# Performance work log

Hardware: AMD Instinct MI355X
Metric: run time of the kernel (lower is better)

The kernel has to match this reference:

```python
import jax, jax.numpy as jnp
import numpy as np
import math

GOLDEN_CENTER = 1.0 / math.e
GOLDEN_LOWER = 0.5 - math.log(4.0 / 3.0)
GOLDEN_UPPER = 0.5

B, T, D = 4, 2048, 1024
E = 8
I = 4096 // (E // 2)  # expert_inter = 1024


def setup_inputs() -> dict:
    key = jax.random.key(0)
    k = jax.random.split(key, 6)
    s_d = 1.0 / math.sqrt(D)
    s_i = 1.0 / math.sqrt(I)
    return {
        "x": jax.random.normal(k[0], (B, T, D), jnp.float32),
        "Wg": jax.random.normal(k[1], (E, D, I), jnp.float32) * s_d,
        "Wu": jax.random.normal(k[2], (E, D, I), jnp.float32) * s_d,
        "Wd": jax.random.normal(k[3], (E, I, D), jnp.float32) * s_i,
        "Wr": jax.random.normal(k[4], (D, E), jnp.float32) * s_d,
        "temperature": jnp.ones((1,), jnp.float32),
    }


def _routing_weights(x, Wr, temperature):
    # inhibition: [B,T,E]
    inh = jax.nn.sigmoid((x @ Wr) / temperature)
    in_zone = (inh >= GOLDEN_LOWER) & (inh <= GOLDEN_UPPER)
    dist = jnp.abs(inh - GOLDEN_CENTER)
    w = jnp.exp(-dist / 0.1) * in_zone.astype(x.dtype)
    wsum = w.sum(axis=-1, keepdims=True)
    no_expert = wsum < 1e-8
    # fallback: softer decay, keep top-2 experts, renormalize
    fb = jnp.exp(-dist / 0.3)
    _, top2 = jax.lax.top_k(fb, 2)  # [B,T,2]
    fb_mask = jax.nn.one_hot(top2, E, dtype=x.dtype).sum(axis=-2)  # [B,T,E]
    fb_w = fb * fb_mask
    fb_w = fb_w / jnp.clip(fb_w.sum(axis=-1, keepdims=True), 1e-8)
    w = jnp.where(no_expert, fb_w, w)
    wsum = w.sum(axis=-1, keepdims=True)
    return w / jnp.clip(wsum, 1e-8)


def reference(x, Wg, Wu, Wd, Wr, temperature):
    weights = _routing_weights(x, Wr, temperature)  # [B,T,E]
    gate = jnp.einsum("btd,edi->beti", x, Wg)
    up = jnp.einsum("btd,edi->beti", x, Wu)
    h = jax.nn.silu(gate) * up  # [B,E,T,I]
    e_out = jnp.einsum("beti,eid->betd", h, Wd)
    out = jnp.einsum("bte,betd->btd", weights, e_out)
    return out
```

## Files before the change

kernel.cpp:

```cpp
#include <hip/hip_runtime.h>
#include <hip/hip_bf16.h>
#include <cstdint>

typedef __attribute__((ext_vector_type(8))) _Float16 f16x8;
typedef __attribute__((ext_vector_type(4))) _Float16 f16x4;
typedef __attribute__((ext_vector_type(4))) float f32x4;

#define GOLDEN_CENTER_F 0.36787944117144233f
#define GOLDEN_LOWER_F  0.21231792754821915f
#define GOLDEN_UPPER_F  0.5f

static constexpr int Dm = 1024;
static constexpr int Im = 1024;
static constexpr int NTOK = 8192;
static constexpr int NE = 8;

__device__ __forceinline__ void async16(const _Float16* g, _Float16* l) {
  __builtin_amdgcn_global_load_lds(
      (const __attribute__((address_space(1))) void*)g,
      (__attribute__((address_space(3))) void*)l,
      16, 0, 0);
}

__global__ void routing_kernel(const float* __restrict__ x, const float* __restrict__ Wr,
                               const float* __restrict__ temp, float* __restrict__ wts) {
  const int wave = threadIdx.x >> 6, lane = threadIdx.x & 63;
  const int t = blockIdx.x * 4 + wave;
  const float* xr = x + (size_t)t * Dm;
  float acc[NE] = {0.f,0.f,0.f,0.f,0.f,0.f,0.f,0.f};
  for (int d = lane; d < Dm; d += 64) {
    float xv = xr[d];
    const float* wr = Wr + (size_t)d * NE;
#pragma unroll
    for (int e = 0; e < NE; ++e) acc[e] += xv * wr[e];
  }
#pragma unroll
  for (int off = 32; off > 0; off >>= 1) {
#pragma unroll
    for (int e = 0; e < NE; ++e) acc[e] += __shfl_down(acc[e], off, 64);
  }
  if (lane == 0) {
    float T = temp[0];
    float w[NE], dist[NE];
    float wsum = 0.f;
#pragma unroll
    for (int e = 0; e < NE; ++e) {
      float inh = 1.f / (1.f + expf(-acc[e] / T));
      dist[e] = fabsf(inh - GOLDEN_CENTER_F);
      bool zone = (inh >= GOLDEN_LOWER_F) && (inh <= GOLDEN_UPPER_F);
      w[e] = zone ? expf(-dist[e] / 0.1f) : 0.f;
      wsum += w[e];
    }
    if (wsum < 1e-8f) {
      float fb[NE];
#pragma unroll
      for (int e = 0; e < NE; ++e) fb[e] = expf(-dist[e] / 0.3f);
      int i1 = 0;
      for (int e = 1; e < NE; ++e) if (fb[e] > fb[i1]) i1 = e;
      int i2 = (i1 == 0) ? 1 : 0;
      for (int e = 0; e < NE; ++e) if (e != i1 && fb[e] > fb[i2]) i2 = e;
      float s = fmaxf(fb[i1] + fb[i2], 1e-8f);
#pragma unroll
      for (int e = 0; e < NE; ++e) w[e] = 0.f;
      w[i1] = fb[i1] / s;
      w[i2] = fb[i2] / s;
      wsum = w[i1] + w[i2];
    }
    float inv = 1.f / fmaxf(wsum, 1e-8f);
#pragma unroll
    for (int e = 0; e < NE; ++e) wts[(size_t)t * NE + e] = w[e] * inv;
  }
}

__global__ void compact_kernel(const float* __restrict__ wts, int* __restrict__ tok,
                               float* __restrict__ wc, int* __restrict__ cnt,
                               int* __restrict__ pos) {
  const int e = blockIdx.x;
  const int tid = threadIdx.x;
  const int wave = tid >> 6, lane = tid & 63;
  __shared__ int wcnt[4];
  __shared__ int s_running;
  if (tid == 0) s_running = 0;
  __syncthreads();
  for (int base = 0; base < NTOK; base += 256) {
    int t = base + tid;
    float w = wts[(size_t)t * NE + e];
    bool act = w > 0.f;
    unsigned long long mask = __ballot(act);
    int prefix = __popcll(mask & ((1ull << lane) - 1ull));
    if (lane == 0) wcnt[wave] = __popcll(mask);
    __syncthreads();
    int wbase = 0;
    for (int i = 0; i < wave; ++i) wbase += wcnt[i];
    int run = s_running;
    int p = run + wbase + prefix;
    pos[(size_t)t * NE + e] = act ? p : -1;
    if (act) {
      tok[(size_t)e * NTOK + p] = t;
      wc[(size_t)e * NTOK + p] = w;
    }
    __syncthreads();
    if (tid == 0) s_running = run + wcnt[0] + wcnt[1] + wcnt[2] + wcnt[3];
    __syncthreads();
  }
  int c = s_running;
  if (tid == 0) cnt[e] = c;
  int padded = (c + 127) & ~127;
  for (int p = c + tid; p < padded; p += 256) {
    tok[(size_t)e * NTOK + p] = 0;
    wc[(size_t)e * NTOK + p] = 0.f;
  }
}

__global__ void cvt_x_kernel(const float* __restrict__ x, _Float16* __restrict__ xb) {
  size_t i = ((size_t)blockIdx.x * 256 + threadIdx.x) * 4;
  float4 v = *(const float4*)(x + i);
  f16x4 o = {(_Float16)v.x, (_Float16)v.y, (_Float16)v.z, (_Float16)v.w};
  *(f16x4*)(xb + i) = o;
}

__global__ void transpose_cvt_kernel(const float* __restrict__ Wg, const float* __restrict__ Wu,
                                     const float* __restrict__ Wd, _Float16* __restrict__ WgT,
                                     _Float16* __restrict__ WuT, _Float16* __restrict__ WdT) {
  __shared__ float tile[32][33];
  const int which = blockIdx.z >> 3;
  const int e = blockIdx.z & 7;
  const float* src = which == 0 ? Wg : which == 1 ? Wu : Wd;
  _Float16* dst = which == 0 ? WgT : which == 1 ? WuT : WdT;
  const size_t base = (size_t)e * 1024 * 1024;
  const int r0 = blockIdx.y * 32, c0 = blockIdx.x * 32;
  const int tx = threadIdx.x & 31, ty = threadIdx.x >> 5;
#pragma unroll
  for (int j = 0; j < 32; j += 8)
    tile[ty + j][tx] = src[base + (size_t)(r0 + ty + j) * 1024 + c0 + tx];
  __syncthreads();
#pragma unroll
  for (int j = 0; j < 32; j += 8)
    dst[base + (size_t)(c0 + ty + j) * 1024 + r0 + tx] = (_Float16)tile[tx][ty + j];
}

__global__ __launch_bounds__(256, 2) void gemm1_kernel(
    const _Float16* __restrict__ A, const _Float16* __restrict__ BgAll,
    const _Float16* __restrict__ BuAll, const int* __restrict__ tok,
    const int* __restrict__ cnt, _Float16* __restrict__ hbuf, int ebase) {
  constexpr int K = Dm;
  const int z = blockIdx.z;
  const int e = ebase + z;
  const int r0 = blockIdx.y * 128;
  if (r0 >= cnt[e]) return;
  const int n0 = blockIdx.x * 128;
  const _Float16* Bg = BgAll + (size_t)e * Dm * Im;
  const _Float16* Bu = BuAll + (size_t)e * Dm * Im;
  _Float16* H = hbuf + (size_t)z * NTOK * Im;
  const int* tk = tok + (size_t)e * NTOK;

  __shared__ _Float16 As[128 * 32];
  __shared__ _Float16 Bgs[128 * 32];
  __shared__ _Float16 Bus[128 * 32];
  const int tid = threadIdx.x;
  const int wave = tid >> 6, lane = tid & 63;
  const int m_off = (wave & 1) * 64, n_off = (wave >> 1) * 64;

  f32x4 accg[4][4], accu[4][4];
#pragma unroll
  for (int i = 0; i < 4; ++i)
#pragma unroll
    for (int j = 0; j < 4; ++j) { accg[i][j] = (f32x4)0.f; accu[i][j] = (f32x4)0.f; }

  const int srow = lane >> 2;
  const int scol = (lane & 3) * 8;
  const int ridx = r0 + wave * 32 + srow;
  const int tA0 = tk[ridx];
  const int tA1 = tk[ridx + 16];
  const _Float16* gA0 = A + (size_t)tA0 * K + scol;
  const _Float16* gA1 = A + (size_t)tA1 * K + scol;
  const _Float16* gBg = Bg + (size_t)(n0 + wave * 32 + srow) * K + scol;
  const _Float16* gBu = Bu + (size_t)(n0 + wave * 32 + srow) * K + scol;
  _Float16* lA  = As  + (wave * 32) * 32;
  _Float16* lBg = Bgs + (wave * 32) * 32;
  _Float16* lBu = Bus + (wave * 32) * 32;

  const int fr = lane & 15, fq = lane >> 4;
  const int aoff = (m_off + fr) * 32 + fq * 8;
  const int boff = (n_off + fr) * 32 + fq * 8;

  for (int k0 = 0; k0 < K; k0 += 32) {
    __syncthreads();
    async16(gA0 + k0, lA);
    async16(gA1 + k0, lA + 16 * 32);
    async16(gBg + k0, lBg);
    async16(gBg + k0 + 16 * K, lBg + 16 * 32);
    async16(gBu + k0, lBu);
    async16(gBu + k0 + 16 * K, lBu + 16 * 32);
    __syncthreads();

    f16x8 af[4], bgf[4], buf2[4];
#pragma unroll
    for (int i = 0; i < 4; ++i) {
      af[i]   = *(const f16x8*)(As  + aoff + i * 16 * 32);
      bgf[i]  = *(const f16x8*)(Bgs + boff + i * 16 * 32);
      buf2[i] = *(const f16x8*)(Bus + boff + i * 16 * 32);
    }
#pragma unroll
    for (int im = 0; im < 4; ++im)
#pragma unroll
      for (int in2 = 0; in2 < 4; ++in2) {
        accg[im][in2] = __builtin_amdgcn_mfma_f32_16x16x32_f16(af[im], bgf[in2], accg[im][in2], 0, 0, 0);
        accu[im][in2] = __builtin_amdgcn_mfma_f32_16x16x32_f16(af[im], buf2[in2], accu[im][in2], 0, 0, 0);
      }
  }

#pragma unroll
  for (int im = 0; im < 4; ++im)
#pragma unroll
    for (int in2 = 0; in2 < 4; ++in2)
#pragma unroll
      for (int r = 0; r < 4; ++r) {
        int row = r0 + m_off + im * 16 + fq * 4 + r;
        int c = n0 + n_off + in2 * 16 + fr;
        float g = accg[im][in2][r], u = accu[im][in2][r];
        float s = g / (1.f + __expf(-g));
        H[(size_t)row * Im + c] = (_Float16)(s * u);
      }
}

__global__ __launch_bounds__(256, 2) void gemm2_kernel(
    const _Float16* __restrict__ hbuf, const _Float16* __restrict__ BAll,
    const int* __restrict__ cnt, _Float16* __restrict__ ebuf, int ebase) {
  constexpr int K = Im;
  const int z = blockIdx.z;
  const int e = ebase + z;
  const int r0 = blockIdx.y * 128;
  if (r0 >= cnt[e]) return;
  const int n0 = blockIdx.x * 128;
  const _Float16* A = hbuf + (size_t)z * NTOK * Im;
  const _Float16* B = BAll + (size_t)e * Im * Dm;
  _Float16* Ez = ebuf + (size_t)z * NTOK * Dm;

  __shared__ _Float16 As[128 * 32];
  __shared__ _Float16 Bs[128 * 32];
  const int tid = threadIdx.x;
  const int wave = tid >> 6, lane = tid & 63;
  const int m_off = (wave & 1) * 64, n_off = (wave >> 1) * 64;

  f32x4 acc[4][4];
#pragma unroll
  for (int i = 0; i < 4; ++i)
#pragma unroll
    for (int j = 0; j < 4; ++j) acc[i][j] = (f32x4)0.f;

  const int srow = lane >> 2;
  const int scol = (lane & 3) * 8;
  const _Float16* gA = A + (size_t)(r0 + wave * 32 + srow) * K + scol;
  const _Float16* gB = B + (size_t)(n0 + wave * 32 + srow) * K + scol;
  _Float16* lA = As + (wave * 32) * 32;
  _Float16* lB = Bs + (wave * 32) * 32;

  const int fr = lane & 15, fq = lane >> 4;
  const int aoff = (m_off + fr) * 32 + fq * 8;
  const int boff = (n_off + fr) * 32 + fq * 8;

  for (int k0 = 0; k0 < K; k0 += 32) {
    __syncthreads();
    async16(gA + k0, lA);
    async16(gA + k0 + 16 * K, lA + 16 * 32);
    async16(gB + k0, lB);
    async16(gB + k0 + 16 * K, lB + 16 * 32);
    __syncthreads();

    f16x8 af[4], bf[4];
#pragma unroll
    for (int i = 0; i < 4; ++i) {
      af[i] = *(const f16x8*)(As + aoff + i * 16 * 32);
      bf[i] = *(const f16x8*)(Bs + boff + i * 16 * 32);
    }
#pragma unroll
    for (int im = 0; im < 4; ++im)
#pragma unroll
      for (int in2 = 0; in2 < 4; ++in2)
        acc[im][in2] = __builtin_amdgcn_mfma_f32_16x16x32_f16(af[im], bf[in2], acc[im][in2], 0, 0, 0);
  }

#pragma unroll
  for (int im = 0; im < 4; ++im)
#pragma unroll
    for (int in2 = 0; in2 < 4; ++in2)
#pragma unroll
      for (int r = 0; r < 4; ++r) {
        int row = m_off + im * 16 + fq * 4 + r;
        int c = n0 + n_off + in2 * 16 + fr;
        Ez[((size_t)(r0 + row)) * Dm + c] = (_Float16)acc[im][in2][r];
      }
}

__global__ void combine_kernel(const _Float16* __restrict__ ebuf, const int* __restrict__ pos,
                               const float* __restrict__ wts, float* __restrict__ out,
                               int ebase, int g, int accum) {
  const int t = blockIdx.x;
  __shared__ int sp[NE];
  __shared__ float sw[NE];
  if (threadIdx.x < g) {
    sp[threadIdx.x] = pos[(size_t)t * NE + ebase + threadIdx.x];
    sw[threadIdx.x] = wts[(size_t)t * NE + ebase + threadIdx.x];
  }
  __syncthreads();
  const int c = threadIdx.x * 4;
  float4 s;
  if (accum) s = *(const float4*)(out + (size_t)t * Dm + c);
  else s = float4{0.f, 0.f, 0.f, 0.f};
  for (int j = 0; j < g; ++j) {
    int p = sp[j];
    if (p >= 0) {
      float w = sw[j];
      f16x4 v = *(const f16x4*)(ebuf + ((size_t)j * NTOK + p) * Dm + c);
      s.x += w * (float)v[0];
      s.y += w * (float)v[1];
      s.z += w * (float)v[2];
      s.w += w * (float)v[3];
    }
  }
  *(float4*)(out + (size_t)t * Dm + c) = s;
}

extern "C" void kernel_launch(void* const* d_in, const int* in_sizes, int n_in,
                              void* d_out, int out_size, void* d_ws, size_t ws_size,
                              hipStream_t stream) {
  const float* x    = (const float*)d_in[0];
  const float* Wg   = (const float*)d_in[1];
  const float* Wu   = (const float*)d_in[2];
  const float* Wd   = (const float*)d_in[3];
  const float* Wr   = (const float*)d_in[4];
  const float* temp = (const float*)d_in[5];
  float* out = (float*)d_out;

  char* ws = (char*)d_ws;
  size_t off = 0;
  auto carve = [&](size_t bytes) {
    char* p = ws + off;
    off = (off + bytes + 255) & ~(size_t)255;
    return p;
  };
  float* wts = (float*)carve((size_t)NTOK * NE * 4);
  int*   tok = (int*)  carve((size_t)NE * NTOK * 4);
  float* wc  = (float*)carve((size_t)NE * NTOK * 4);
  int*   pos = (int*)  carve((size_t)NTOK * NE * 4);
  int*   cnt = (int*)  carve(4096);
  _Float16* xb   = (_Float16*)carve((size_t)NTOK * Dm * 2);
  _Float16* WgT  = (_Float16*)carve((size_t)NE * Dm * Im * 2);
  _Float16* WuT  = (_Float16*)carve((size_t)NE * Dm * Im * 2);
  _Float16* WdT  = (_Float16*)carve((size_t)NE * Dm * Im * 2);
  const size_t fixed_off = off;
  const size_t per_expert = (size_t)NTOK * Im * 2 + (size_t)NTOK * Dm * 2;
  int g = (ws_size >= fixed_off + 8 * per_expert) ? 8 : 4;
  _Float16* hbuf = (_Float16*)carve((size_t)g * NTOK * Im * 2);
  _Float16* ebuf = (_Float16*)carve((size_t)g * NTOK * Dm * 2);

  routing_kernel<<<NTOK / 4, 256, 0, stream>>>(x, Wr, temp, wts);
  compact_kernel<<<NE, 256, 0, stream>>>(wts, tok, wc, cnt, pos);
  cvt_x_kernel<<<(NTOK * Dm) / 1024, 256, 0, stream>>>(x, xb);
  transpose_cvt_kernel<<<dim3(32, 32, 24), 256, 0, stream>>>(Wg, Wu, Wd, WgT, WuT, WdT);

  for (int e0 = 0; e0 < NE; e0 += g) {
    gemm1_kernel<<<dim3(Im / 128, NTOK / 128, g), 256, 0, stream>>>(xb, WgT, WuT, tok, cnt, hbuf, e0);
    gemm2_kernel<<<dim3(Dm / 128, NTOK / 128, g), 256, 0, stream>>>(hbuf, WdT, cnt, ebuf, e0);
    combine_kernel<<<NTOK, 256, 0, stream>>>(ebuf, pos, wts, out, e0, g, e0 > 0);
  }
}
```

Baseline: 488.9 us.

## Double-buffer LDS tiles and XOR-swizzle layout in both expert GEMMs

Both grouped GEMM kernels now keep two LDS buffers and issue the async global-to-LDS loads for the next K tile before computing on the current one. Explicit vmcnt waits and barriers replace the two __syncthreads per iteration, so load latency can overlap with MFMA work. The 16-byte column chunks are also XOR-swizzled by row in the loads and fragment reads, to reduce LDS bank conflicts. LDS use per block doubles, which may reduce occupancy. The hand-written waitcnt counts depend on the compiler not reordering or adding other memory ops.

Result: no change. 483.9 us (-1.0%).

```diff
diff --git a/kernel.cpp b/kernel.cpp
--- a/kernel.cpp
+++ b/kernel.cpp
@@ -154,9 +154,9 @@
   _Float16* H = hbuf + (size_t)z * NTOK * Im;
   const int* tk = tok + (size_t)e * NTOK;
 
-  __shared__ _Float16 As[128 * 32];
-  __shared__ _Float16 Bgs[128 * 32];
-  __shared__ _Float16 Bus[128 * 32];
+  __shared__ _Float16 As[2][128 * 32];
+  __shared__ _Float16 Bgs[2][128 * 32];
+  __shared__ _Float16 Bus[2][128 * 32];
   const int tid = threadIdx.x;
   const int wave = tid >> 6, lane = tid & 63;
   const int m_off = (wave & 1) * 64, n_off = (wave >> 1) * 64;
@@ -168,7 +168,7 @@
     for (int j = 0; j < 4; ++j) { accg[i][j] = (f32x4)0.f; accu[i][j] = (f32x4)0.f; }
 
   const int srow = lane >> 2;
-  const int scol = (lane & 3) * 8;
+  const int scol = ((lane & 3) ^ ((srow >> 1) & 3)) * 8;
   const int ridx = r0 + wave * 32 + srow;
   const int tA0 = tk[ridx];
   const int tA1 = tk[ridx + 16];
@@ -176,30 +176,43 @@
   const _Float16* gA1 = A + (size_t)tA1 * K + scol;
   const _Float16* gBg = Bg + (size_t)(n0 + wave * 32 + srow) * K + scol;
   const _Float16* gBu = Bu + (size_t)(n0 + wave * 32 + srow) * K + scol;
-  _Float16* lA  = As  + (wave * 32) * 32;
-  _Float16* lBg = Bgs + (wave * 32) * 32;
-  _Float16* lBu = Bus + (wave * 32) * 32;
+  const int lbase = (wave * 32) * 32;
 
   const int fr = lane & 15, fq = lane >> 4;
-  const int aoff = (m_off + fr) * 32 + fq * 8;
-  const int boff = (n_off + fr) * 32 + fq * 8;
-
-  for (int k0 = 0; k0 < K; k0 += 32) {
-    __syncthreads();
-    async16(gA0 + k0, lA);
-    async16(gA1 + k0, lA + 16 * 32);
-    async16(gBg + k0, lBg);
-    async16(gBg + k0 + 16 * K, lBg + 16 * 32);
-    async16(gBu + k0, lBu);
-    async16(gBu + k0 + 16 * K, lBu + 16 * 32);
-    __syncthreads();
-
+  const int sw = (fq ^ ((fr >> 1) & 3)) * 8;
+  const int aoff = (m_off + fr) * 32 + sw;
+  const int boff = (n_off + fr) * 32 + sw;
+
+  auto STAGE = [&](int b, int k0) {
+    _Float16* a = &As[b][lbase];
+    _Float16* g = &Bgs[b][lbase];
+    _Float16* u = &Bus[b][lbase];
+    async16(gA0 + k0, a);
+    async16(gA1 + k0, a + 512);
+    async16(gBg + k0, g);
+    async16(gBg + k0 + 16 * K, g + 512);
+    async16(gBu + k0, u);
+    async16(gBu + k0 + 16 * K, u + 512);
+  };
+
+  STAGE(0, 0);
+  for (int t = 0; t < K / 32; ++t) {
+    const int cur = t & 1;
+    if (t + 1 < K / 32) {
+      STAGE(cur ^ 1, (t + 1) * 32);
+      asm volatile("s_waitcnt vmcnt(6)\n\ts_barrier" ::: "memory");
+    } else {
+      asm volatile("s_waitcnt vmcnt(0)\n\ts_barrier" ::: "memory");
+    }
+    const _Float16* Ac = As[cur];
+    const _Float16* Gc = Bgs[cur];
+    const _Float16* Uc = Bus[cur];
     f16x8 af[4], bgf[4], buf2[4];
 #pragma unroll
     for (int i = 0; i < 4; ++i) {
-      af[i]   = *(const f16x8*)(As  + aoff + i * 16 * 32);
-      bgf[i]  = *(const f16x8*)(Bgs + boff + i * 16 * 32);
-      buf2[i] = *(const f16x8*)(Bus + boff + i * 16 * 32);
+      af[i]   = *(const f16x8*)(Ac + aoff + i * 512);
+      bgf[i]  = *(const f16x8*)(Gc + boff + i * 512);
+      buf2[i] = *(const f16x8*)(Uc + boff + i * 512);
     }
 #pragma unroll
     for (int im = 0; im < 4; ++im)
@@ -208,6 +221,7 @@
         accg[im][in2] = __builtin_amdgcn_mfma_f32_16x16x32_f16(af[im], bgf[in2], accg[im][in2], 0, 0, 0);
         accu[im][in2] = __builtin_amdgcn_mfma_f32_16x16x32_f16(af[im], buf2[in2], accu[im][in2], 0, 0, 0);
       }
+    asm volatile("s_waitcnt lgkmcnt(0)\n\ts_barrier" ::: "memory");
   }
 
 #pragma unroll
@@ -237,8 +251,8 @@
   const _Float16* B = BAll + (size_t)e * Im * Dm;
   _Float16* Ez = ebuf + (size_t)z * NTOK * Dm;
 
-  __shared__ _Float16 As[128 * 32];
-  __shared__ _Float16 Bs[128 * 32];
+  __shared__ _Float16 As[2][128 * 32];
+  __shared__ _Float16 Bs[2][128 * 32];
   const int tid = threadIdx.x;
   const int wave = tid >> 6, lane = tid & 63;
   const int m_off = (wave & 1) * 64, n_off = (wave >> 1) * 64;
@@ -250,35 +264,48 @@
     for (int j = 0; j < 4; ++j) acc[i][j] = (f32x4)0.f;
 
   const int srow = lane >> 2;
-  const int scol = (lane & 3) * 8;
+  const int scol = ((lane & 3) ^ ((srow >> 1) & 3)) * 8;
   const _Float16* gA = A + (size_t)(r0 + wave * 32 + srow) * K + scol;
   const _Float16* gB = B + (size_t)(n0 + wave * 32 + srow) * K + scol;
-  _Float16* lA = As + (wave * 32) * 32;
-  _Float16* lB = Bs + (wave * 32) * 32;
+  const int lbase = (wave * 32) * 32;
 
   const int fr = lane & 15, fq = lane >> 4;
-  const int aoff = (m_off + fr) * 32 + fq * 8;
-  const int boff = (n_off + fr) * 32 + fq * 8;
-
-  for (int k0 = 0; k0 < K; k0 += 32) {
-    __syncthreads();
-    async16(gA + k0, lA);
-    async16(gA + k0 + 16 * K, lA + 16 * 32);
-    async16(gB + k0, lB);
-    async16(gB + k0 + 16 * K, lB + 16 * 32);
-    __syncthreads();
-
+  const int sw = (fq ^ ((fr >> 1) & 3)) * 8;
+  const int aoff = (m_off + fr) * 32 + sw;
+  const int boff = (n_off + fr) * 32 + sw;
+
+  auto STAGE = [&](int b, int k0) {
+    _Float16* a = &As[b][lbase];
+    _Float16* bb = &Bs[b][lbase];
+    async16(gA + k0, a);
+    async16(gA + k0 + 16 * K, a + 512);
+    async16(gB + k0, bb);
+    async16(gB + k0 + 16 * K, bb + 512);
+  };
+
+  STAGE(0, 0);
+  for (int t = 0; t < K / 32; ++t) {
+    const int cur = t & 1;
+    if (t + 1 < K / 32) {
+      STAGE(cur ^ 1, (t + 1) * 32);
+      asm volatile("s_waitcnt vmcnt(4)\n\ts_barrier" ::: "memory");
+    } else {
+      asm volatile("s_waitcnt vmcnt(0)\n\ts_barrier" ::: "memory");
+    }
+    const _Float16* Ac = As[cur];
+    const _Float16* Bc = Bs[cur];
     f16x8 af[4], bf[4];
 #pragma unroll
     for (int i = 0; i < 4; ++i) {
-      af[i] = *(const f16x8*)(As + aoff + i * 16 * 32);
-      bf[i] = *(const f16x8*)(Bs + boff + i * 16 * 32);
+      af[i] = *(const f16x8*)(Ac + aoff + i * 512);
+      bf[i] = *(const f16x8*)(Bc + boff + i * 512);
     }
 #pragma unroll
     for (int im = 0; im < 4; ++im)
 #pragma unroll
       for (int in2 = 0; in2 < 4; ++in2)
         acc[im][in2] = __builtin_amdgcn_mfma_f32_16x16x32_f16(af[im], bf[in2], acc[im][in2], 0, 0, 0);
+    asm volatile("s_waitcnt lgkmcnt(0)\n\ts_barrier" ::: "memory");
   }
 
 #pragma unroll
```

## Rewrite expert GEMMs with 256x256 tiles, double-buffered LDS, swizzle, interleaved gate/up

Applied to the files above, without the earlier changes.

The gate and up weights are interleaved into one [2048 x D] matrix per expert in 16-column groups, so one GEMM computes both and the SiLU*up epilogue pairs adjacent column blocks. Both GEMMs move to 512-thread blocks with 256x256 tiles. They use double-buffered LDS with an XOR swizzle, issue the next tile's async prefetch between MFMA phases, and raise wave priority around the MFMA bursts. The aim is to hide global load latency, cut LDS bank conflicts and raise data reuse, at the cost of much more LDS (128KB), more registers and more padding waste since routed token counts are now padded to 256.

After: 482.0 us. Within noise of the previous version (-1.4%).

```diff
diff --git a/kernel.cpp b/kernel.cpp
--- a/kernel.cpp
+++ b/kernel.cpp
@@ -105,7 +105,7 @@
   }
   int c = s_running;
   if (tid == 0) cnt[e] = c;
-  int padded = (c + 127) & ~127;
+  int padded = (c + 255) & ~255;
   for (int p = c + tid; p < padded; p += 256) {
     tok[(size_t)e * NTOK + p] = 0;
     wc[(size_t)e * NTOK + p] = 0.f;
@@ -120,177 +120,302 @@
 }
 
 __global__ void transpose_cvt_kernel(const float* __restrict__ Wg, const float* __restrict__ Wu,
-                                     const float* __restrict__ Wd, _Float16* __restrict__ WgT,
-                                     _Float16* __restrict__ WuT, _Float16* __restrict__ WdT) {
+                                     const float* __restrict__ Wd, _Float16* __restrict__ Wgu,
+                                     _Float16* __restrict__ WdT) {
   __shared__ float tile[32][33];
   const int which = blockIdx.z >> 3;
   const int e = blockIdx.z & 7;
   const float* src = which == 0 ? Wg : which == 1 ? Wu : Wd;
-  _Float16* dst = which == 0 ? WgT : which == 1 ? WuT : WdT;
-  const size_t base = (size_t)e * 1024 * 1024;
+  const size_t sbase = (size_t)e * 1024 * 1024;
   const int r0 = blockIdx.y * 32, c0 = blockIdx.x * 32;
   const int tx = threadIdx.x & 31, ty = threadIdx.x >> 5;
 #pragma unroll
   for (int j = 0; j < 32; j += 8)
-    tile[ty + j][tx] = src[base + (size_t)(r0 + ty + j) * 1024 + c0 + tx];
+    tile[ty + j][tx] = src[sbase + (size_t)(r0 + ty + j) * 1024 + c0 + tx];
   __syncthreads();
 #pragma unroll
-  for (int j = 0; j < 32; j += 8)
-    dst[base + (size_t)(c0 + ty + j) * 1024 + r0 + tx] = (_Float16)tile[tx][ty + j];
-}
-
-__global__ __launch_bounds__(256, 2) void gemm1_kernel(
-    const _Float16* __restrict__ A, const _Float16* __restrict__ BgAll,
-    const _Float16* __restrict__ BuAll, const int* __restrict__ tok,
-    const int* __restrict__ cnt, _Float16* __restrict__ hbuf, int ebase) {
+  for (int j = 0; j < 32; j += 8) {
+    const int c = c0 + ty + j;
+    float v = tile[tx][ty + j];
+    if (which == 2) {
+      WdT[sbase + (size_t)c * 1024 + r0 + tx] = (_Float16)v;
+    } else {
+      const int n = ((c >> 4) << 5) + (which << 4) + (c & 15);
+      Wgu[(size_t)e * 2048 * 1024 + (size_t)n * 1024 + r0 + tx] = (_Float16)v;
+    }
+  }
+}
+
+
+#define OPEN_PHASE() do { \
+    asm volatile("s_barrier\n\ts_waitcnt lgkmcnt(0)" ::: "memory"); \
+    __builtin_amdgcn_sched_barrier(0); \
+    __builtin_amdgcn_s_setprio(1); \
+  } while (0)
+#define CLOSE_PHASE() do { \
+    __builtin_amdgcn_s_setprio(0); \
+    asm volatile("s_barrier" ::: "memory"); \
+  } while (0)
+#define CLOSE_PHASE_VM(pf) do { \
+    __builtin_amdgcn_s_setprio(0); \
+    if (pf) asm volatile("s_waitcnt vmcnt(4)\n\ts_barrier" ::: "memory"); \
+    else    asm volatile("s_waitcnt vmcnt(0)\n\ts_barrier" ::: "memory"); \
+  } while (0)
+
+__global__ __launch_bounds__(512, 2) void gemm1_kernel(
+    const _Float16* __restrict__ A, const _Float16* __restrict__ Bgu,
+    const int* __restrict__ tok, const int* __restrict__ cnt,
+    _Float16* __restrict__ hbuf, int ebase) {
   constexpr int K = Dm;
+  constexpr int NT = K / 64;
   const int z = blockIdx.z;
   const int e = ebase + z;
-  const int r0 = blockIdx.y * 128;
+  const int r0 = blockIdx.y * 256;
   if (r0 >= cnt[e]) return;
-  const int n0 = blockIdx.x * 128;
-  const _Float16* Bg = BgAll + (size_t)e * Dm * Im;
-  const _Float16* Bu = BuAll + (size_t)e * Dm * Im;
+  const int n0 = blockIdx.x * 256;
+  const _Float16* Bm = Bgu + (size_t)e * 2048 * Dm;
   _Float16* H = hbuf + (size_t)z * NTOK * Im;
   const int* tk = tok + (size_t)e * NTOK;
 
-  __shared__ _Float16 As[128 * 32];
-  __shared__ _Float16 Bgs[128 * 32];
-  __shared__ _Float16 Bus[128 * 32];
+  __shared__ _Float16 sA[2 * 2 * 8192];
+  __shared__ _Float16 sB[2 * 2 * 8192];
+
   const int tid = threadIdx.x;
-  const int wave = tid >> 6, lane = tid & 63;
-  const int m_off = (wave & 1) * 64, n_off = (wave >> 1) * 64;
-
-  f32x4 accg[4][4], accu[4][4];
-#pragma unroll
-  for (int i = 0; i < 4; ++i)
-#pragma unroll
-    for (int j = 0; j < 4; ++j) { accg[i][j] = (f32x4)0.f; accu[i][j] = (f32x4)0.f; }
-
-  const int srow = lane >> 2;
-  const int scol = (lane & 3) * 8;
-  const int ridx = r0 + wave * 32 + srow;
-  const int tA0 = tk[ridx];
-  const int tA1 = tk[ridx + 16];
-  const _Float16* gA0 = A + (size_t)tA0 * K + scol;
-  const _Float16* gA1 = A + (size_t)tA1 * K + scol;
-  const _Float16* gBg = Bg + (size_t)(n0 + wave * 32 + srow) * K + scol;
-  const _Float16* gBu = Bu + (size_t)(n0 + wave * 32 + srow) * K + scol;
-  _Float16* lA  = As  + (wave * 32) * 32;
-  _Float16* lBg = Bgs + (wave * 32) * 32;
-  _Float16* lBu = Bus + (wave * 32) * 32;
+  const int lane = tid & 63;
+  const int w = tid >> 6;
+  const int wm = w >> 2, wn = w & 3;
+
+  const int srow0 = tid >> 2;
+  const int lcc = (tid & 3) ^ ((tid >> 3) & 3);
+  const _Float16* pA0 = A + (size_t)tk[r0 + srow0] * K + lcc * 8;
+  const _Float16* pA1 = A + (size_t)tk[r0 + 128 + srow0] * K + lcc * 8;
+  const _Float16* pB0 = Bm + (size_t)(n0 + srow0) * K + lcc * 8;
+  const _Float16* pB1 = Bm + (size_t)(n0 + 128 + srow0) * K + lcc * 8;
+
+  auto stageA = [&](int buf, int kh, int tile) {
+    const int ko = tile * 64 + kh * 32;
+    _Float16* d = sA + buf * 16384 + kh * 8192 + tid * 8;
+    async16(pA0 + ko, d);
+    async16(pA1 + ko, d + 4096);
+  };
+  auto stageB = [&](int buf, int kh, int tile) {
+    const int ko = tile * 64 + kh * 32;
+    _Float16* d = sB + buf * 16384 + kh * 8192 + tid * 8;
+    async16(pB0 + ko, d);
+    async16(pB1 + ko, d + 4096);
+  };
 
   const int fr = lane & 15, fq = lane >> 4;
-  const int aoff = (m_off + fr) * 32 + fq * 8;
-  const int boff = (n_off + fr) * 32 + fq * 8;
-
-  for (int k0 = 0; k0 < K; k0 += 32) {
-    __syncthreads();
-    async16(gA0 + k0, lA);
-    async16(gA1 + k0, lA + 16 * 32);
-    async16(gBg + k0, lBg);
-    async16(gBg + k0 + 16 * K, lBg + 16 * 32);
-    async16(gBu + k0, lBu);
-    async16(gBu + k0 + 16 * K, lBu + 16 * 32);
-    __syncthreads();
-
-    f16x8 af[4], bgf[4], buf2[4];
-#pragma unroll
-    for (int i = 0; i < 4; ++i) {
-      af[i]   = *(const f16x8*)(As  + aoff + i * 16 * 32);
-      bgf[i]  = *(const f16x8*)(Bgs + boff + i * 16 * 32);
-      buf2[i] = *(const f16x8*)(Bus + boff + i * 16 * 32);
-    }
-#pragma unroll
-    for (int im = 0; im < 4; ++im)
-#pragma unroll
-      for (int in2 = 0; in2 < 4; ++in2) {
-        accg[im][in2] = __builtin_amdgcn_mfma_f32_16x16x32_f16(af[im], bgf[in2], accg[im][in2], 0, 0, 0);
-        accu[im][in2] = __builtin_amdgcn_mfma_f32_16x16x32_f16(af[im], buf2[in2], accu[im][in2], 0, 0, 0);
+  const int sw = (fq ^ ((fr >> 1) & 3)) * 8;
+  const int aro = (wm * 128 + fr) * 32 + sw;
+  const int bro = (wn * 64 + fr) * 32 + sw;
+
+  f32x4 acc[8][4];
+#pragma unroll
+  for (int i = 0; i < 8; ++i)
+#pragma unroll
+    for (int j = 0; j < 4; ++j) acc[i][j] = (f32x4)0.f;
+
+  stageA(0, 0, 0); stageB(0, 0, 0); stageA(0, 1, 0); stageB(0, 1, 0);
+  asm volatile("s_waitcnt vmcnt(4)\n\ts_barrier" ::: "memory");
+
+  f16x8 af[4], bf[4];
+  for (int t = 0; t < NT; ++t) {
+    const int p = t & 1, np = p ^ 1;
+    const bool pf = (t + 1 < NT);
+    const _Float16* Ab = sA + p * 16384;
+    const _Float16* Bb = sB + p * 16384;
+
+#pragma unroll
+    for (int i = 0; i < 4; ++i) bf[i] = *(const f16x8*)(Bb + bro + i * 512);
+#pragma unroll
+    for (int i = 0; i < 4; ++i) af[i] = *(const f16x8*)(Ab + aro + i * 512);
+    if (pf) stageA(np, 0, t + 1);
+    OPEN_PHASE();
+#pragma unroll
+    for (int im = 0; im < 4; ++im)
+#pragma unroll
+      for (int in = 0; in < 4; ++in)
+        acc[im][in] = __builtin_amdgcn_mfma_f32_16x16x32_f16(af[im], bf[in], acc[im][in], 0, 0, 0);
+    CLOSE_PHASE();
+
+#pragma unroll
+    for (int i = 0; i < 4; ++i) af[i] = *(const f16x8*)(Ab + aro + (i + 4) * 512);
+    if (pf) stageB(np, 0, t + 1);
+    OPEN_PHASE();
+#pragma unroll
+    for (int im = 0; im < 4; ++im)
+#pragma unroll
+      for (int in = 0; in < 4; ++in)
+        acc[im + 4][in] = __builtin_amdgcn_mfma_f32_16x16x32_f16(af[im], bf[in], acc[im + 4][in], 0, 0, 0);
+    CLOSE_PHASE_VM(pf);
+
+#pragma unroll
+    for (int i = 0; i < 4; ++i) bf[i] = *(const f16x8*)(Bb + 8192 + bro + i * 512);
+#pragma unroll
+    for (int i = 0; i < 4; ++i) af[i] = *(const f16x8*)(Ab + 8192 + aro + i * 512);
+    if (pf) stageA(np, 1, t + 1);
+    OPEN_PHASE();
+#pragma unroll
+    for (int im = 0; im < 4; ++im)
+#pragma unroll
+      for (int in = 0; in < 4; ++in)
+        acc[im][in] = __builtin_amdgcn_mfma_f32_16x16x32_f16(af[im], bf[in], acc[im][in], 0, 0, 0);
+    CLOSE_PHASE();
+
+#pragma unroll
+    for (int i = 0; i < 4; ++i) af[i] = *(const f16x8*)(Ab + 8192 + aro + (i + 4) * 512);
+    if (pf) stageB(np, 1, t + 1);
+    OPEN_PHASE();
+#pragma unroll
+    for (int im = 0; im < 4; ++im)
+#pragma unroll
+      for (int in = 0; in < 4; ++in)
+        acc[im + 4][in] = __builtin_amdgcn_mfma_f32_16x16x32_f16(af[im], bf[in], acc[im + 4][in], 0, 0, 0);
+    CLOSE_PHASE_VM(pf);
+  }
+
+  const int hc0 = (n0 + wn * 64) >> 1;
+#pragma unroll
+  for (int im = 0; im < 8; ++im) {
+    const int growb = r0 + wm * 128 + im * 16 + fq * 4;
+#pragma unroll
+    for (int pr = 0; pr < 2; ++pr) {
+      const int hcol = hc0 + pr * 16 + fr;
+#pragma unroll
+      for (int r = 0; r < 4; ++r) {
+        float g = acc[im][pr * 2][r];
+        float u = acc[im][pr * 2 + 1][r];
+        float s = g / (1.f + __expf(-g));
+        H[(size_t)(growb + r) * Im + hcol] = (_Float16)(s * u);
       }
-  }
-
-#pragma unroll
-  for (int im = 0; im < 4; ++im)
-#pragma unroll
-    for (int in2 = 0; in2 < 4; ++in2)
-#pragma unroll
-      for (int r = 0; r < 4; ++r) {
-        int row = r0 + m_off + im * 16 + fq * 4 + r;
-        int c = n0 + n_off + in2 * 16 + fr;
-        float g = accg[im][in2][r], u = accu[im][in2][r];
-        float s = g / (1.f + __expf(-g));
-        H[(size_t)row * Im + c] = (_Float16)(s * u);
-      }
-}
-
-__global__ __launch_bounds__(256, 2) void gemm2_kernel(
-    const _Float16* __restrict__ hbuf, const _Float16* __restrict__ BAll,
+    }
+  }
+}
+
+__global__ __launch_bounds__(512, 2) void gemm2_kernel(
+    const _Float16* __restrict__ hb, const _Float16* __restrict__ BAll,
     const int* __restrict__ cnt, _Float16* __restrict__ ebuf, int ebase) {
   constexpr int K = Im;
+  constexpr int NT = K / 64;
   const int z = blockIdx.z;
   const int e = ebase + z;
-  const int r0 = blockIdx.y * 128;
+  const int r0 = blockIdx.y * 256;
   if (r0 >= cnt[e]) return;
-  const int n0 = blockIdx.x * 128;
-  const _Float16* A = hbuf + (size_t)z * NTOK * Im;
-  const _Float16* B = BAll + (size_t)e * Im * Dm;
+  const int n0 = blockIdx.x * 256;
+  const _Float16* A = hb + (size_t)z * NTOK * Im;
+  const _Float16* Bm = BAll + (size_t)e * Im * Dm;
   _Float16* Ez = ebuf + (size_t)z * NTOK * Dm;
 
-  __shared__ _Float16 As[128 * 32];
-  __shared__ _Float16 Bs[128 * 32];
+  __shared__ _Float16 sA[2 * 2 * 8192];
+  __shared__ _Float16 sB[2 * 2 * 8192];
+
   const int tid = threadIdx.x;
-  const int wave = tid >> 6, lane = tid & 63;
-  const int m_off = (wave & 1) * 64, n_off = (wave >> 1) * 64;
-
-  f32x4 acc[4][4];
-#pragma unroll
-  for (int i = 0; i < 4; ++i)
+  const int lane = tid & 63;
+  const int w = tid >> 6;
+  const int wm = w >> 2, wn = w & 3;
+
+  const int srow0 = tid >> 2;
+  const int lcc = (tid & 3) ^ ((tid >> 3) & 3);
+  const _Float16* pA0 = A + (size_t)(r0 + srow0) * K + lcc * 8;
+  const _Float16* pA1 = A + (size_t)(r0 + 128 + srow0) * K + lcc * 8;
+  const _Float16* pB0 = Bm + (size_t)(n0 + srow0) * K + lcc * 8;
+  const _Float16* pB1 = Bm + (size_t)(n0 + 128 + srow0) * K + lcc * 8;
+
+  auto stageA = [&](int buf, int kh, int tile) {
+    const int ko = tile * 64 + kh * 32;
+    _Float16* d = sA + buf * 16384 + kh * 8192 + tid * 8;
+    async16(pA0 + ko, d);
+    async16(pA1 + ko, d + 4096);
+  };
+  auto stageB = [&](int buf, int kh, int tile) {
+    const int ko = tile * 64 + kh * 32;
+    _Float16* d = sB + buf * 16384 + kh * 8192 + tid * 8;
+    async16(pB0 + ko, d);
+    async16(pB1 + ko, d + 4096);
+  };
+
+  const int fr = lane & 15, fq = lane >> 4;
+  const int sw = (fq ^ ((fr >> 1) & 3)) * 8;
+  const int aro = (wm * 128 + fr) * 32 + sw;
+  const int bro = (wn * 64 + fr) * 32 + sw;
+
+  f32x4 acc[8][4];
+#pragma unroll
+  for (int i = 0; i < 8; ++i)
 #pragma unroll
     for (int j = 0; j < 4; ++j) acc[i][j] = (f32x4)0.f;
 
-  const int srow = lane >> 2;
-  const int scol = (lane & 3) * 8;
-  const _Float16* gA = A + (size_t)(r0 + wave * 32 + srow) * K + scol;
-  const _Float16* gB = B + (size_t)(n0 + wave * 32 + srow) * K + scol;
-  _Float16* lA = As + (wave * 32) * 32;
-  _Float16* lB = Bs + (wave * 32) * 32;
-
-  const int fr = lane & 15, fq = lane >> 4;
-  const int aoff = (m_off + fr) * 32 + fq * 8;
-  const int boff = (n_off + fr) * 32 + fq * 8;
-
-  for (int k0 = 0; k0 < K; k0 += 32) {
-    __syncthreads();
-    async16(gA + k0, lA);
-    async16(gA + k0 + 16 * K, lA + 16 * 32);
-    async16(gB + k0, lB);
-    async16(gB + k0 + 16 * K, lB + 16 * 32);
-    __syncthreads();
-
-    f16x8 af[4], bf[4];
-#pragma unroll
-    for (int i = 0; i < 4; ++i) {
-      af[i] = *(const f16x8*)(As + aoff + i * 16 * 32);
-      bf[i] = *(const f16x8*)(Bs + boff + i * 16 * 32);
-    }
-#pragma unroll
-    for (int im = 0; im < 4; ++im)
-#pragma unroll
-      for (int in2 = 0; in2 < 4; ++in2)
-        acc[im][in2] = __builtin_amdgcn_mfma_f32_16x16x32_f16(af[im], bf[in2], acc[im][in2], 0, 0, 0);
-  }
-
-#pragma unroll
-  for (int im = 0; im < 4; ++im)
-#pragma unroll
-    for (int in2 = 0; in2 < 4; ++in2)
-#pragma unroll
-      for (int r = 0; r < 4; ++r) {
-        int row = m_off + im * 16 + fq * 4 + r;
-        int c = n0 + n_off + in2 * 16 + fr;
-        Ez[((size_t)(r0 + row)) * Dm + c] = (_Float16)acc[im][in2][r];
-      }
+  stageA(0, 0, 0); stageB(0, 0, 0); stageA(0, 1, 0); stageB(0, 1, 0);
+  asm volatile("s_waitcnt vmcnt(4)\n\ts_barrier" ::: "memory");
+
+  f16x8 af[4], bf[4];
+  for (int t = 0; t < NT; ++t) {
+    const int p = t & 1, np = p ^ 1;
+    const bool pf = (t + 1 < NT);
+    const _Float16* Ab = sA + p * 16384;
+    const _Float16* Bb = sB + p * 16384;
+
+#pragma unroll
+    for (int i = 0; i < 4; ++i) bf[i] = *(const f16x8*)(Bb + bro + i * 512);
+#pragma unroll
+    for (int i = 0; i < 4; ++i) af[i] = *(const f16x8*)(Ab + aro + i * 512);
+    if (pf) stageA(np, 0, t + 1);
+    OPEN_PHASE();
+#pragma unroll
+    for (int im = 0; im < 4; ++im)
+#pragma unroll
+      for (int in = 0; in < 4; ++in)
+        acc[im][in] = __builtin_amdgcn_mfma_f32_16x16x32_f16(af[im], bf[in], acc[im][in], 0, 0, 0);
+    CLOSE_PHASE();
+
+#pragma unroll
+    for (int i = 0; i < 4; ++i) af[i] = *(const f16x8*)(Ab + aro + (i + 4) * 512);
+    if (pf) stageB(np, 0, t + 1);
+    OPEN_PHASE();
+#pragma unroll
+    for (int im = 0; im < 4; ++im)
+#pragma unroll
+      for (int in = 0; in < 4; ++in)
+        acc[im + 4][in] = __builtin_amdgcn_mfma_f32_16x16x32_f16(af[im], bf[in], acc[im + 4][in], 0, 0, 0);
+    CLOSE_PHASE_VM(pf);
+
+#pragma unroll
+    for (int i = 0; i < 4; ++i) bf[i] = *(const f16x8*)(Bb + 8192 + bro + i * 512);
+#pragma unroll
+    for (int i = 0; i < 4; ++i) af[i] = *(const f16x8*)(Ab + 8192 + aro + i * 512);
+    if (pf) stageA(np, 1, t + 1);
+    OPEN_PHASE();
+#pragma unroll
+    for (int im = 0; im < 4; ++im)
+#pragma unroll
+      for (int in = 0; in < 4; ++in)
+        acc[im][in] = __builtin_amdgcn_mfma_f32_16x16x32_f16(af[im], bf[in], acc[im][in], 0, 0, 0);
+    CLOSE_PHASE();
+
+#pragma unroll
+    for (int i = 0; i < 4; ++i) af[i] = *(const f16x8*)(Ab + 8192 + aro + (i + 4) * 512);
+    if (pf) stageB(np, 1, t + 1);
+    OPEN_PHASE();
+#pragma unroll
+    for (int im = 0; im < 4; ++im)
+#pragma unroll
+      for (int in = 0; in < 4; ++in)
+        acc[im + 4][in] = __builtin_amdgcn_mfma_f32_16x16x32_f16(af[im], bf[in], acc[im + 4][in], 0, 0, 0);
+    CLOSE_PHASE_VM(pf);
+  }
+
+#pragma unroll
+  for (int im = 0; im < 8; ++im) {
+    const int growb = r0 + wm * 128 + im * 16 + fq * 4;
+#pragma unroll
+    for (int in = 0; in < 4; ++in) {
+      const int col = n0 + wn * 64 + in * 16 + fr;
+#pragma unroll
+      for (int r = 0; r < 4; ++r)
+        Ez[(size_t)(growb + r) * Dm + col] = (_Float16)acc[im][in][r];
+    }
+  }
 }
 
 __global__ void combine_kernel(const _Float16* __restrict__ ebuf, const int* __restrict__ pos,
@@ -298,10 +423,10 @@
                                int ebase, int g, int accum) {
   const int t = blockIdx.x;
   __shared__ int sp[NE];
-  __shared__ float sw[NE];
+  __shared__ float swt[NE];
   if (threadIdx.x < g) {
     sp[threadIdx.x] = pos[(size_t)t * NE + ebase + threadIdx.x];
-    sw[threadIdx.x] = wts[(size_t)t * NE + ebase + threadIdx.x];
+    swt[threadIdx.x] = wts[(size_t)t * NE + ebase + threadIdx.x];
   }
   __syncthreads();
   const int c = threadIdx.x * 4;
@@ -311,7 +436,7 @@
   for (int j = 0; j < g; ++j) {
     int p = sp[j];
     if (p >= 0) {
-      float w = sw[j];
+      float w = swt[j];
       f16x4 v = *(const f16x4*)(ebuf + ((size_t)j * NTOK + p) * Dm + c);
       s.x += w * (float)v[0];
       s.y += w * (float)v[1];
@@ -346,9 +471,8 @@
   int*   pos = (int*)  carve((size_t)NTOK * NE * 4);
   int*   cnt = (int*)  carve(4096);
   _Float16* xb   = (_Float16*)carve((size_t)NTOK * Dm * 2);
-  _Float16* WgT  = (_Float16*)carve((size_t)NE * Dm * Im * 2);
-  _Float16* WuT  = (_Float16*)carve((size_t)NE * Dm * Im * 2);
-  _Float16* WdT  = (_Float16*)carve((size_t)NE * Dm * Im * 2);
+  _Float16* Wgu  = (_Float16*)carve((size_t)NE * 2048 * Dm * 2);
+  _Float16* WdT  = (_Float16*)carve((size_t)NE * Im * Dm * 2);
   const size_t fixed_off = off;
   const size_t per_expert = (size_t)NTOK * Im * 2 + (size_t)NTOK * Dm * 2;
   int g = (ws_size >= fixed_off + 8 * per_expert) ? 8 : 4;
@@ -358,11 +482,11 @@
   routing_kernel<<<NTOK / 4, 256, 0, stream>>>(x, Wr, temp, wts);
   compact_kernel<<<NE, 256, 0, stream>>>(wts, tok, wc, cnt, pos);
   cvt_x_kernel<<<(NTOK * Dm) / 1024, 256, 0, stream>>>(x, xb);
-  transpose_cvt_kernel<<<dim3(32, 32, 24), 256, 0, stream>>>(Wg, Wu, Wd, WgT, WuT, WdT);
+  transpose_cvt_kernel<<<dim3(32, 32, 24), 256, 0, stream>>>(Wg, Wu, Wd, Wgu, WdT);
 
   for (int e0 = 0; e0 < NE; e0 += g) {
-    gemm1_kernel<<<dim3(Im / 128, NTOK / 128, g), 256, 0, stream>>>(xb, WgT, WuT, tok, cnt, hbuf, e0);
-    gemm2_kernel<<<dim3(Dm / 128, NTOK / 128, g), 256, 0, stream>>>(hbuf, WdT, cnt, ebuf, e0);
+    gemm1_kernel<<<dim3(2048 / 256, NTOK / 256, g), 512, 0, stream>>>(xb, Wgu, tok, cnt, hbuf, e0);
+    gemm2_kernel<<<dim3(Dm / 256, NTOK / 256, g), 512, 0, stream>>>(hbuf, WdT, cnt, ebuf, e0);
     combine_kernel<<<NTOK, 256, 0, stream>>>(ebuf, pos, wts, out, e0, g, e0 > 0);
   }
 }
```
